# Optimization experiments

Measured on AMD Instinct MI355X. Metric: run time of the kernel, lower is better.

## Reference

```python
import jax, jax.numpy as jnp
import numpy as np

NUM_HEADS = 20
MAX_SEQLEN = 1500  # max per-segment length (Whisper 30s -> 1500 frames); static for jit
NEG = -1e30


def setup_inputs() -> dict:
    key = jax.random.key(0)
    ks = jax.random.split(key, 6)
    B, S, D = 4, MAX_SEQLEN, 1280
    T = B * S
    hidden_states = jax.random.normal(ks[0], (T, D), dtype=jnp.float32)
    # packed varlen layout: 4 equal-length audio segments
    cu_seqlens = (jnp.arange(B + 1, dtype=jnp.int32) * S)
    w = 0.02
    Wq = jax.random.normal(ks[1], (D, D), dtype=jnp.float32) * w
    Wk = jax.random.normal(ks[2], (D, D), dtype=jnp.float32) * w
    Wv = jax.random.normal(ks[3], (D, D), dtype=jnp.float32) * w
    Wo = jax.random.normal(ks[4], (D, D), dtype=jnp.float32) * w
    bq = jnp.zeros((D,), jnp.float32)
    bv = jnp.zeros((D,), jnp.float32)
    bo = jnp.zeros((D,), jnp.float32)
    return {"hidden_states": hidden_states, "cu_seqlens": cu_seqlens,
            "Wq": Wq, "bq": bq, "Wk": Wk, "Wv": Wv, "bv": bv, "Wo": Wo, "bo": bo}


def _varlen_attention(hidden_states, cu_seqlens, Wq, bq, Wk, Wv, bv, Wo, bo):
    T, D = hidden_states.shape
    H = NUM_HEADS
    d = D // H
    scale = d ** -0.5
    S = MAX_SEQLEN
    B = cu_seqlens.shape[0] - 1

    # projections (torch nn.Linear convention: y = x @ W.T + b; k_proj has no bias)
    q = hidden_states @ Wq.T + bq   # [T, D]
    k = hidden_states @ Wk.T        # [T, D]
    v = hidden_states @ Wv.T + bv   # [T, D]

    lens = cu_seqlens[1:] - cu_seqlens[:-1]                 # [B]
    pos = jnp.arange(S, dtype=jnp.int32)                    # [S]
    valid = pos[None, :] < lens[:, None]                    # [B, S]
    idx = cu_seqlens[:-1, None] + pos[None, :]              # [B, S]
    idx_g = jnp.where(valid, idx, 0)

    # unpack to padded [B, S, H, d]
    qb = q[idx_g].reshape(B, S, H, d)
    kb = k[idx_g].reshape(B, S, H, d)
    vb = v[idx_g].reshape(B, S, H, d)

    scores = jnp.einsum('bqhd,bkhd->bhqk', qb, kb) * scale  # [B, H, S, S]
    scores = jnp.where(valid[:, None, None, :], scores, NEG)
    attn = jax.nn.softmax(scores, axis=-1)
    out = jnp.einsum('bhqk,bkhd->bqhd', attn, vb).reshape(B, S, D)

    # repack to [T, D]; invalid slots scatter out-of-bounds and are dropped
    idx_s = jnp.where(valid, idx, T).reshape(-1)
    packed = jnp.zeros((T, D), out.dtype).at[idx_s].set(out.reshape(-1, D), mode='drop')
    return packed @ Wo.T + bo


def reference(hidden_states, cu_seqlens, Wq, bq, Wk, Wv, bv, Wo, bo):
    return _varlen_attention(hidden_states, cu_seqlens, Wq, bq, Wk, Wv, bv, Wo, bo)
```

## Files before the change

### kernel.cpp

```cpp
#include <hip/hip_runtime.h>
#include <stdint.h>
#include <math.h>

#define DMODEL 1280
#define NHEAD  20
#define DHEAD  64
#define NSEG   4
#define MAXS   1500
#define SPAD   1536
#define TPAD   (NSEG*SPAD)
#define QT128  ((MAXS + 127) / 128)
#define ST64   ((MAXS + 63) / 64)
#define BM 128
#define BN 128
#define BK 32
#define QSCALE 0.18033688011112042f
#define NEGV  -1e30f

typedef float  f32x4  __attribute__((ext_vector_type(4)));
typedef __bf16 bf16x8 __attribute__((ext_vector_type(8)));

__device__ __forceinline__ ushort f2bf(float f) {
  union { float f; uint32_t u; } a; a.f = f;
  uint32_t u = a.u;
  u += 0x7FFFu + ((u >> 16) & 1u);
  return (ushort)(u >> 16);
}

__device__ __forceinline__ uint32_t pk2(float a, float b) {
  union { float f; uint32_t u; } ua, ub; ua.f = a; ub.f = b;
  uint32_t x = ua.u + 0x8000u, y = ub.u + 0x8000u;
  return (x >> 16) | (y & 0xFFFF0000u);
}

__device__ __forceinline__ void async16(const void* g, void* lds) {
  __builtin_amdgcn_global_load_lds((const __attribute__((address_space(1))) void*)g,
                                   (__attribute__((address_space(3))) void*)lds,
                                   16, 0, 0);
}

__device__ __forceinline__ int perm32(int a) {
  return ((a >> 2) & 3) * 8 + ((a >> 4) & 1) * 4 + (a & 3);
}

__global__ void __launch_bounds__(256)
cvt_bf16(const float* __restrict__ src, ushort* __restrict__ dst, int n) {
  int i = (blockIdx.x * 256 + threadIdx.x) * 4;
  if (i >= n) return;
  float4 v = *(const float4*)(src + i);
  ushort4 o;
  o.x = f2bf(v.x); o.y = f2bf(v.y); o.z = f2bf(v.z); o.w = f2bf(v.w);
  *(ushort4*)(dst + i) = o;
}

__global__ void __launch_bounds__(256)
cvt_w4(const float* __restrict__ Wq, const float* __restrict__ Wk,
       const float* __restrict__ Wv, const float* __restrict__ Wo,
       ushort* __restrict__ dst, int DD) {
  const int z = blockIdx.y;
  const float* src = (z == 0) ? Wq : (z == 1) ? Wk : (z == 2) ? Wv : Wo;
  int i = (blockIdx.x * 256 + threadIdx.x) * 4;
  if (i >= DD) return;
  float4 v = *(const float4*)(src + i);
  ushort4 o;
  o.x = f2bf(v.x); o.y = f2bf(v.y); o.z = f2bf(v.z); o.w = f2bf(v.w);
  *(ushort4*)(dst + (size_t)z * DD + i) = o;
}

__device__ __forceinline__ void gemm_tile_mainloop(
    const ushort* __restrict__ A, const ushort* __restrict__ W,
    int M, int m0, int n0, ushort* As, ushort* Bs, f32x4 (&acc)[4][4])
{
  const int tid  = threadIdx.x;
  const int wave = tid >> 6, lane = tid & 63;
  const int quad = lane >> 4, c16 = lane & 15;
  const int wr = (wave >> 1) * 64, wc = (wave & 1) * 64;

  const int e0 = (wave * 2 + 0) * 512 + lane * 8;
  const int e1 = (wave * 2 + 1) * 512 + lane * 8;
  const int M0 = e0 >> 3, M1 = e1 >> 3;
  const int ra0 = M0 >> 2, ra1 = M1 >> 2;
  const int ca0 = (((M0 & 3) ^ (ra0 & 3) ^ ((ra0 >> 2) & 3)) << 3);
  const int ca1 = (((M1 & 3) ^ (ra1 & 3) ^ ((ra1 >> 2) & 3)) << 3);
  int ga0 = m0 + ra0; if (ga0 > M - 1) ga0 = M - 1;
  int ga1 = m0 + ra1; if (ga1 > M - 1) ga1 = M - 1;
  const ushort* Ap0 = A + (size_t)ga0 * DMODEL + ca0;
  const ushort* Ap1 = A + (size_t)ga1 * DMODEL + ca1;
  const ushort* Bp0 = W + (size_t)(n0 + ra0) * DMODEL + ca0;
  const ushort* Bp1 = W + (size_t)(n0 + ra1) * DMODEL + ca1;
  const int o0 = (wave * 2 + 0) * 512;
  const int o1 = (wave * 2 + 1) * 512;
  const int BUF = BM * BK;

  const int sw = (c16 & 3) ^ ((c16 >> 2) & 3);

  async16(Ap0, As + o0); async16(Ap1, As + o1);
  async16(Bp0, Bs + o0); async16(Bp1, Bs + o1);

  int c = 0;
  for (int k0 = 0; k0 < DMODEL; k0 += BK, c ^= 1) {
    __syncthreads();
    if (k0 + BK < DMODEL) {
      const int kn = k0 + BK;
      const int bo = (c ^ 1) * BUF;
      async16(Ap0 + kn, As + bo + o0); async16(Ap1 + kn, As + bo + o1);
      async16(Bp0 + kn, Bs + bo + o0); async16(Bp1 + kn, Bs + bo + o1);
    }
    const ushort* Ab = As + c * BUF;
    const ushort* Bb = Bs + c * BUF;
    bf16x8 a[4], b[4];
#pragma unroll
    for (int i = 0; i < 4; ++i)
      a[i] = *(const bf16x8*)(Ab + (wr + i * 16 + c16) * BK + ((quad ^ sw) << 3));
#pragma unroll
    for (int j = 0; j < 4; ++j)
      b[j] = *(const bf16x8*)(Bb + (wc + j * 16 + c16) * BK + ((quad ^ sw) << 3));
#pragma unroll
    for (int i = 0; i < 4; ++i)
#pragma unroll
      for (int j = 0; j < 4; ++j)
        acc[i][j] = __builtin_amdgcn_mfma_f32_16x16x32_bf16(a[i], b[j], acc[i][j], 0, 0, 0);
  }
}

__global__ void __launch_bounds__(256, 2)
gemm_qkv(const ushort* __restrict__ X, const ushort* __restrict__ W4,
         const float* __restrict__ bq, const float* __restrict__ bv,
         ushort* __restrict__ qb, ushort* __restrict__ kb, ushort* __restrict__ vb, int M)
{
  __shared__ ushort As[2 * BM * BK], Bs[2 * BN * BK];
  const int wg = blockIdx.x;
  if (wg >= 30) return;
  const int z = wg / 10;
  const int n0 = (wg % 10) * BN;
  const int m0 = blockIdx.y * BM;
  const ushort* W = W4 + (size_t)z * DMODEL * DMODEL;
  ushort* out = (z == 0) ? qb : ((z == 1) ? kb : vb);
  const float* bias = (z == 0) ? bq : ((z == 2) ? bv : (const float*)nullptr);
  const float oscale = (z == 0) ? QSCALE : 1.0f;

  f32x4 acc[4][4];
  f32x4 zero = {0.f, 0.f, 0.f, 0.f};
#pragma unroll
  for (int i = 0; i < 4; ++i)
#pragma unroll
    for (int j = 0; j < 4; ++j) acc[i][j] = zero;

  gemm_tile_mainloop(X, W, M, m0, n0, As, Bs, acc);

  const int tid = threadIdx.x, wave = tid >> 6, lane = tid & 63;
  const int quad = lane >> 4, c16 = lane & 15;
  const int wr = (wave >> 1) * 64, wc = (wave & 1) * 64;
#pragma unroll
  for (int i = 0; i < 4; ++i) {
    const int rbase = m0 + wr + i * 16 + quad * 4;
#pragma unroll
    for (int j = 0; j < 4; ++j) {
      const int c = n0 + wc + j * 16 + c16;
      const float bb = bias ? bias[c] : 0.f;
#pragma unroll
      for (int r = 0; r < 4; ++r) {
        const int rr = rbase + r;
        if (rr < M) out[(size_t)rr * DMODEL + c] = f2bf((acc[i][j][r] + bb) * oscale);
      }
    }
  }
}

__global__ void __launch_bounds__(256, 2)
gemm_out(const ushort* __restrict__ A, const ushort* __restrict__ W,
         const float* __restrict__ bias, float* __restrict__ out, int M)
{
  __shared__ ushort As[2 * BM * BK], Bs[2 * BN * BK];
  const int wg = blockIdx.x;
  if (wg >= 10) return;
  const int n0 = wg * BN;
  const int m0 = blockIdx.y * BM;
  f32x4 acc[4][4];
  f32x4 zero = {0.f, 0.f, 0.f, 0.f};
#pragma unroll
  for (int i = 0; i < 4; ++i)
#pragma unroll
    for (int j = 0; j < 4; ++j) acc[i][j] = zero;

  gemm_tile_mainloop(A, W, M, m0, n0, As, Bs, acc);

  const int tid = threadIdx.x, wave = tid >> 6, lane = tid & 63;
  const int quad = lane >> 4, c16 = lane & 15;
  const int wr = (wave >> 1) * 64, wc = (wave & 1) * 64;
#pragma unroll
  for (int i = 0; i < 4; ++i) {
    const int rbase = m0 + wr + i * 16 + quad * 4;
#pragma unroll
    for (int j = 0; j < 4; ++j) {
      const int c = n0 + wc + j * 16 + c16;
      const float bb = bias[c];
#pragma unroll
      for (int r = 0; r < 4; ++r) {
        const int rr = rbase + r;
        if (rr < M) out[(size_t)rr * DMODEL + c] = acc[i][j][r] + bb;
      }
    }
  }
}

__global__ void __launch_bounds__(256)
transpose_v(const ushort* __restrict__ vb, ushort* __restrict__ vt,
            const int* __restrict__ cu, int T)
{
  __shared__ ushort tile[64][72];
  const int bseg = blockIdx.z;
  const int seg0 = cu[bseg], len = cu[bseg + 1] - seg0;
  const int s0 = blockIdx.x * 64;
  if (s0 >= len) return;
  const int d0 = blockIdx.y * 64;
  const int tid = threadIdx.x;
#pragma unroll
  for (int i = 0; i < 2; ++i) {
    const int e = i * 2048 + tid * 8;
    const int r = e >> 6, c = e & 63;
    int t = seg0 + s0 + r;
    if (t > seg0 + len - 1) t = seg0 + len - 1;
    uint4 v = *(const uint4*)(vb + (size_t)t * DMODEL + d0 + c);
    *(uint4*)(&tile[r][c]) = v;
  }
  __syncthreads();
#pragma unroll
  for (int i = 0; i < 2; ++i) {
    const int e = i * 2048 + tid * 8;
    const int c = e >> 6;
    const int r = e & 63;
    const int s = s0 + r;
    ushort tmp[8];
#pragma unroll
    for (int j = 0; j < 8; ++j) tmp[j] = tile[r + j][c];
    const int o = r & 31;
    const size_t rowbase = (size_t)(d0 + c) * TPAD + (size_t)bseg * SPAD + (size_t)(s & ~31);
    if (s + 7 < len) {
      const int p0 = perm32(o), p1 = perm32(o + 4);
      uint2 w0, w1;
      w0.x = (uint32_t)tmp[0] | ((uint32_t)tmp[1] << 16);
      w0.y = (uint32_t)tmp[2] | ((uint32_t)tmp[3] << 16);
      w1.x = (uint32_t)tmp[4] | ((uint32_t)tmp[5] << 16);
      w1.y = (uint32_t)tmp[6] | ((uint32_t)tmp[7] << 16);
      *(uint2*)(vt + rowbase + p0) = w0;
      *(uint2*)(vt + rowbase + p1) = w1;
    } else {
#pragma unroll
      for (int j = 0; j < 8; ++j)
        if (s + j < len) vt[rowbase + perm32(o + j)] = tmp[j];
    }
  }
}

__global__ void __launch_bounds__(256, 2)
attn_fused(const ushort* __restrict__ qb, const ushort* __restrict__ kb,
           const ushort* __restrict__ vt, ushort* __restrict__ ob,
           const int* __restrict__ cu, int T)
{
  __shared__ ushort Qs[128 * 64];
  __shared__ ushort Ks[2][64 * 64];
  __shared__ ushort Vs[2][64 * 64];
  const int hs = blockIdx.x;
  const int b = hs / NHEAD, h = hs % NHEAD;
  const int seg0 = cu[b];
  const int len  = cu[b + 1] - seg0;
  const int q0 = blockIdx.y * 128;
  if (q0 >= len) return;
  const int tid = threadIdx.x, wave = tid >> 6, lane = tid & 63;
  const int quad = lane >> 4, c16 = lane & 15;

#pragma unroll
  for (int t = 0; t < 4; ++t) {
    const int M = t * 256 + wave * 64 + lane;
    const int r = M >> 3, k2 = M & 7;
    const int col = ((k2 ^ (r & 7)) << 3);
    int qr = q0 + r; if (qr >= len) qr = len - 1;
    async16(qb + (size_t)(seg0 + qr) * DMODEL + h * DHEAD + col,
            Qs + (t * 256 + wave * 64) * 8);
  }

  const int niter = (len + 63) >> 6;
#pragma unroll
  for (int t = 0; t < 2; ++t) {
    const int M = t * 256 + wave * 64 + lane;
    const int r = M >> 3, k2 = M & 7;
    const int col = ((k2 ^ (r & 7)) << 3);
    int rr = r; if (rr > len - 1) rr = len - 1;
    async16(kb + (size_t)(seg0 + rr) * DMODEL + h * DHEAD + col,
            Ks[0] + (t * 256 + wave * 64) * 8);
    async16(vt + (size_t)(h * DHEAD + r) * TPAD + (size_t)b * SPAD + col,
            Vs[0] + (t * 256 + wave * 64) * 8);
  }

  bf16x8 aq[2][2];
  float l_i[2] = {0.f, 0.f};
  f32x4 o_acc[2][4];
  f32x4 zero = {0.f, 0.f, 0.f, 0.f};
#pragma unroll
  for (int n = 0; n < 2; ++n)
#pragma unroll
    for (int m = 0; m < 4; ++m) o_acc[n][m] = zero;

  for (int it = 0; it < niter; ++it) {
    const int kv0 = it * 64;
    const int c = it & 1;
    __syncthreads();

    if (it + 1 < niter) {
      const int kvn = kv0 + 64;
      const int lim = len - 1 - kvn;
#pragma unroll
      for (int t = 0; t < 2; ++t) {
        const int M = t * 256 + wave * 64 + lane;
        const int r = M >> 3, k2 = M & 7;
        const int col = ((k2 ^ (r & 7)) << 3);
        int rr = r; if (rr > lim) rr = lim;
        async16(kb + (size_t)(seg0 + kvn + rr) * DMODEL + h * DHEAD + col,
                Ks[c ^ 1] + (t * 256 + wave * 64) * 8);
        async16(vt + (size_t)(h * DHEAD + r) * TPAD + (size_t)b * SPAD + kvn + col,
                Vs[c ^ 1] + (t * 256 + wave * 64) * 8);
      }
    }

    if (it == 0) {
#pragma unroll
      for (int n = 0; n < 2; ++n)
#pragma unroll
        for (int ks = 0; ks < 2; ++ks) {
          const int row = wave * 32 + n * 16 + c16;
          aq[n][ks] = *(const bf16x8*)(Qs + row * 64 + (((ks * 4 + quad) ^ (c16 & 7)) << 3));
        }
    }

    f32x4 s[2][4];
#pragma unroll
    for (int f = 0; f < 4; ++f) {
      const int row = f * 16 + c16;
      const int ch = c16 & 7;
      bf16x8 ak0 = *(const bf16x8*)(Ks[c] + row * 64 + ((quad ^ ch) << 3));
      bf16x8 ak1 = *(const bf16x8*)(Ks[c] + row * 64 + (((4 + quad) ^ ch) << 3));
#pragma unroll
      for (int n = 0; n < 2; ++n) {
        s[n][f] = zero;
        s[n][f] = __builtin_amdgcn_mfma_f32_16x16x32_bf16(ak0, aq[n][0], s[n][f], 0, 0, 0);
        s[n][f] = __builtin_amdgcn_mfma_f32_16x16x32_bf16(ak1, aq[n][1], s[n][f], 0, 0, 0);
      }
    }

    if (kv0 + 64 > len) {
#pragma unroll
      for (int f = 0; f < 4; ++f) {
        const int kvb = kv0 + f * 16 + quad * 4;
#pragma unroll
        for (int r = 0; r < 4; ++r)
          if (kvb + r >= len) { s[0][f][r] = NEGV; s[1][f][r] = NEGV; }
      }
    }

#pragma unroll
    for (int n = 0; n < 2; ++n) {
      float rs = 0.f;
#pragma unroll
      for (int f = 0; f < 4; ++f)
#pragma unroll
        for (int r = 0; r < 4; ++r) {
          const float p = exp2f(s[n][f][r]);
          s[n][f][r] = p;
          rs += p;
        }
      l_i[n] += rs;
    }

    bf16x8 bp[2][2];
#pragma unroll
    for (int n = 0; n < 2; ++n)
#pragma unroll
      for (int g = 0; g < 2; ++g) {
        union { uint32_t u[4]; bf16x8 v; } cv;
        cv.u[0] = pk2(s[n][2 * g][0], s[n][2 * g][1]);
        cv.u[1] = pk2(s[n][2 * g][2], s[n][2 * g][3]);
        cv.u[2] = pk2(s[n][2 * g + 1][0], s[n][2 * g + 1][1]);
        cv.u[3] = pk2(s[n][2 * g + 1][2], s[n][2 * g + 1][3]);
        bp[n][g] = cv.v;
      }

#pragma unroll
    for (int m = 0; m < 4; ++m) {
      const int row = m * 16 + c16;
      const int ch = c16 & 7;
      bf16x8 av0 = *(const bf16x8*)(Vs[c] + row * 64 + ((quad ^ ch) << 3));
      bf16x8 av1 = *(const bf16x8*)(Vs[c] + row * 64 + (((4 + quad) ^ ch) << 3));
#pragma unroll
      for (int n = 0; n < 2; ++n) {
        o_acc[n][m] = __builtin_amdgcn_mfma_f32_16x16x32_bf16(av0, bp[n][0], o_acc[n][m], 0, 0, 0);
        o_acc[n][m] = __builtin_amdgcn_mfma_f32_16x16x32_bf16(av1, bp[n][1], o_acc[n][m], 0, 0, 0);
      }
    }
  }

#pragma unroll
  for (int n = 0; n < 2; ++n) {
    float l = l_i[n];
    l += __shfl_xor(l, 16);
    l += __shfl_xor(l, 32);
    const int q = q0 + wave * 32 + n * 16 + c16;
    if (q < len) {
      const float inv = 1.0f / l;
      const size_t base = (size_t)(seg0 + q) * DMODEL + h * DHEAD;
#pragma unroll
      for (int m = 0; m < 4; ++m) {
        ushort4 pk;
        pk.x = f2bf(o_acc[n][m][0] * inv);
        pk.y = f2bf(o_acc[n][m][1] * inv);
        pk.z = f2bf(o_acc[n][m][2] * inv);
        pk.w = f2bf(o_acc[n][m][3] * inv);
        *(ushort4*)(ob + base + m * 16 + quad * 4) = pk;
      }
    }
  }
}

extern "C" void kernel_launch(void* const* d_in, const int* in_sizes, int n_in,
                              void* d_out, int out_size, void* d_ws, size_t ws_size,
                              hipStream_t stream)
{
  (void)n_in; (void)out_size; (void)ws_size;
  const float* hs = (const float*)d_in[0];
  const int*   cu = (const int*)d_in[1];
  const float* Wq = (const float*)d_in[2];
  const float* bq = (const float*)d_in[3];
  const float* Wk = (const float*)d_in[4];
  const float* Wv = (const float*)d_in[5];
  const float* bv = (const float*)d_in[6];
  const float* Wo = (const float*)d_in[7];
  const float* bo = (const float*)d_in[8];
  float* out = (float*)d_out;
  const int T  = in_sizes[0] / DMODEL;
  const int DD = DMODEL * DMODEL;

  ushort* ws  = (ushort*)d_ws;
  ushort* vtX = ws;
  const size_t szA = (size_t)DMODEL * TPAD;
  ushort* W4 = vtX + szA;
  ushort* qb = W4 + 4 * (size_t)DD;
  ushort* kb = qb + (size_t)T * DMODEL;
  ushort* vb = kb + (size_t)T * DMODEL;
  ushort* ob = vb;

  const int nX = T * DMODEL;
  cvt_bf16<<<(nX / 4 + 255) / 256, 256, 0, stream>>>(hs, vtX, nX);
  cvt_w4<<<dim3((DD / 4 + 255) / 256, 4), 256, 0, stream>>>(Wq, Wk, Wv, Wo, W4, DD);

  gemm_qkv<<<dim3(32, (T + BM - 1) / BM), 256, 0, stream>>>(vtX, W4, bq, bv, qb, kb, vb, T);

  transpose_v<<<dim3(ST64, DMODEL / 64, NSEG), 256, 0, stream>>>(vb, vtX, cu, T);

  attn_fused<<<dim3(NSEG * NHEAD, QT128), 256, 0, stream>>>(qb, kb, vtX, ob, cu, T);

  gemm_out<<<dim3(16, (T + BM - 1) / BM), 256, 0, stream>>>(
      ob, W4 + 3 * (size_t)DD, bo, out, T);
}
```

Measured before the change: 352.0 us.

## Fuse V transpose into QKV GEMM epilogue, merge convert kernels, retune LDS swizzle

The QKV GEMM epilogue now writes V directly into the permuted, transposed, segment-padded layout that attention consumes, so the separate transpose_v kernel and its round trip through global memory go away. The two fp32-to-bf16 conversion kernels are merged into one launch. The GEMM LDS layout switches to a different XOR swizzle over 64-element super-rows. Launch bounds for the GEMMs and attention are raised to 3 waves-per-SIMD occupancy hints. The V epilogue now does strided scattered stores with per-row segment lookups, and the tighter register budget may cause spills.

```diff
diff --git a/kernel.cpp b/kernel.cpp
--- a/kernel.cpp
+++ b/kernel.cpp
@@ -10,7 +10,6 @@
 #define SPAD   1536
 #define TPAD   (NSEG*SPAD)
 #define QT128  ((MAXS + 127) / 128)
-#define ST64   ((MAXS + 63) / 64)
 #define BM 128
 #define BN 128
 #define BK 32
@@ -44,27 +43,23 @@
 }
 
 __global__ void __launch_bounds__(256)
-cvt_bf16(const float* __restrict__ src, ushort* __restrict__ dst, int n) {
-  int i = (blockIdx.x * 256 + threadIdx.x) * 4;
-  if (i >= n) return;
-  float4 v = *(const float4*)(src + i);
+cvt_all(const float* __restrict__ hs, const float* __restrict__ Wq,
+        const float* __restrict__ Wk, const float* __restrict__ Wv,
+        const float* __restrict__ Wo, ushort* __restrict__ dst, int nX, int DD) {
+  const int i = (blockIdx.x * 256 + threadIdx.x) * 4;
+  const float* src;
+  if (i < nX) {
+    src = hs + i;
+  } else {
+    int j = i - nX;
+    const int z = (j >= DD) + (j >= 2 * DD) + (j >= 3 * DD);
+    const float* w = (z == 0) ? Wq : (z == 1) ? Wk : (z == 2) ? Wv : Wo;
+    src = w + (j - z * DD);
+  }
+  float4 v = *(const float4*)src;
   ushort4 o;
   o.x = f2bf(v.x); o.y = f2bf(v.y); o.z = f2bf(v.z); o.w = f2bf(v.w);
   *(ushort4*)(dst + i) = o;
-}
-
-__global__ void __launch_bounds__(256)
-cvt_w4(const float* __restrict__ Wq, const float* __restrict__ Wk,
-       const float* __restrict__ Wv, const float* __restrict__ Wo,
-       ushort* __restrict__ dst, int DD) {
-  const int z = blockIdx.y;
-  const float* src = (z == 0) ? Wq : (z == 1) ? Wk : (z == 2) ? Wv : Wo;
-  int i = (blockIdx.x * 256 + threadIdx.x) * 4;
-  if (i >= DD) return;
-  float4 v = *(const float4*)(src + i);
-  ushort4 o;
-  o.x = f2bf(v.x); o.y = f2bf(v.y); o.z = f2bf(v.z); o.w = f2bf(v.w);
-  *(ushort4*)(dst + (size_t)z * DD + i) = o;
 }
 
 __device__ __forceinline__ void gemm_tile_mainloop(
@@ -76,23 +71,20 @@
   const int quad = lane >> 4, c16 = lane & 15;
   const int wr = (wave >> 1) * 64, wc = (wave & 1) * 64;
 
-  const int e0 = (wave * 2 + 0) * 512 + lane * 8;
-  const int e1 = (wave * 2 + 1) * 512 + lane * 8;
-  const int M0 = e0 >> 3, M1 = e1 >> 3;
-  const int ra0 = M0 >> 2, ra1 = M1 >> 2;
-  const int ca0 = (((M0 & 3) ^ (ra0 & 3) ^ ((ra0 >> 2) & 3)) << 3);
-  const int ca1 = (((M1 & 3) ^ (ra1 & 3) ^ ((ra1 >> 2) & 3)) << 3);
-  int ga0 = m0 + ra0; if (ga0 > M - 1) ga0 = M - 1;
-  int ga1 = m0 + ra1; if (ga1 > M - 1) ga1 = M - 1;
-  const ushort* Ap0 = A + (size_t)ga0 * DMODEL + ca0;
-  const ushort* Ap1 = A + (size_t)ga1 * DMODEL + ca1;
-  const ushort* Bp0 = W + (size_t)(n0 + ra0) * DMODEL + ca0;
-  const ushort* Bp1 = W + (size_t)(n0 + ra1) * DMODEL + ca1;
-  const int o0 = (wave * 2 + 0) * 512;
-  const int o1 = (wave * 2 + 1) * 512;
+  const int M0 = wave * 128 + lane, M1 = M0 + 64;
+  const int sr0 = M0 >> 3, pp0 = M0 & 7, p0 = pp0 ^ (sr0 & 7);
+  const int sr1 = M1 >> 3, pp1 = M1 & 7, p1 = pp1 ^ (sr1 & 7);
+  const int row0 = sr0 * 2 + (p0 >> 2), kc0 = (p0 & 3) << 3;
+  const int row1 = sr1 * 2 + (p1 >> 2), kc1 = (p1 & 3) << 3;
+  int ga0 = m0 + row0; if (ga0 > M - 1) ga0 = M - 1;
+  int ga1 = m0 + row1; if (ga1 > M - 1) ga1 = M - 1;
+  const ushort* Ap0 = A + (size_t)ga0 * DMODEL + kc0;
+  const ushort* Ap1 = A + (size_t)ga1 * DMODEL + kc1;
+  const ushort* Bp0 = W + (size_t)(n0 + row0) * DMODEL + kc0;
+  const ushort* Bp1 = W + (size_t)(n0 + row1) * DMODEL + kc1;
+  const int o0 = wave * 1024;
+  const int o1 = wave * 1024 + 512;
   const int BUF = BM * BK;
-
-  const int sw = (c16 & 3) ^ ((c16 >> 2) & 3);
 
   async16(Ap0, As + o0); async16(Ap1, As + o1);
   async16(Bp0, Bs + o0); async16(Bp1, Bs + o1);
@@ -110,11 +102,19 @@
     const ushort* Bb = Bs + c * BUF;
     bf16x8 a[4], b[4];
 #pragma unroll
-    for (int i = 0; i < 4; ++i)
-      a[i] = *(const bf16x8*)(Ab + (wr + i * 16 + c16) * BK + ((quad ^ sw) << 3));
-#pragma unroll
-    for (int j = 0; j < 4; ++j)
-      b[j] = *(const bf16x8*)(Bb + (wc + j * 16 + c16) * BK + ((quad ^ sw) << 3));
+    for (int i = 0; i < 4; ++i) {
+      const int row = wr + i * 16 + c16;
+      const int sr = row >> 1;
+      const int off = (sr << 6) + (((((row & 1) << 2) | quad) ^ (sr & 7)) << 3);
+      a[i] = *(const bf16x8*)(Ab + off);
+    }
+#pragma unroll
+    for (int j = 0; j < 4; ++j) {
+      const int row = wc + j * 16 + c16;
+      const int sr = row >> 1;
+      const int off = (sr << 6) + (((((row & 1) << 2) | quad) ^ (sr & 7)) << 3);
+      b[j] = *(const bf16x8*)(Bb + off);
+    }
 #pragma unroll
     for (int i = 0; i < 4; ++i)
 #pragma unroll
@@ -123,10 +123,11 @@
   }
 }
 
-__global__ void __launch_bounds__(256, 2)
+__global__ void __launch_bounds__(256, 3)
 gemm_qkv(const ushort* __restrict__ X, const ushort* __restrict__ W4,
          const float* __restrict__ bq, const float* __restrict__ bv,
-         ushort* __restrict__ qb, ushort* __restrict__ kb, ushort* __restrict__ vb, int M)
+         const int* __restrict__ cu,
+         ushort* __restrict__ qb, ushort* __restrict__ kb, ushort* __restrict__ vt, int M)
 {
   __shared__ ushort As[2 * BM * BK], Bs[2 * BN * BK];
   const int wg = blockIdx.x;
@@ -135,9 +136,6 @@
   const int n0 = (wg % 10) * BN;
   const int m0 = blockIdx.y * BM;
   const ushort* W = W4 + (size_t)z * DMODEL * DMODEL;
-  ushort* out = (z == 0) ? qb : ((z == 1) ? kb : vb);
-  const float* bias = (z == 0) ? bq : ((z == 2) ? bv : (const float*)nullptr);
-  const float oscale = (z == 0) ? QSCALE : 1.0f;
 
   f32x4 acc[4][4];
   f32x4 zero = {0.f, 0.f, 0.f, 0.f};
@@ -151,23 +149,66 @@
   const int tid = threadIdx.x, wave = tid >> 6, lane = tid & 63;
   const int quad = lane >> 4, c16 = lane & 15;
   const int wr = (wave >> 1) * 64, wc = (wave & 1) * 64;
-#pragma unroll
-  for (int i = 0; i < 4; ++i) {
-    const int rbase = m0 + wr + i * 16 + quad * 4;
-#pragma unroll
-    for (int j = 0; j < 4; ++j) {
-      const int c = n0 + wc + j * 16 + c16;
-      const float bb = bias ? bias[c] : 0.f;
-#pragma unroll
-      for (int r = 0; r < 4; ++r) {
-        const int rr = rbase + r;
-        if (rr < M) out[(size_t)rr * DMODEL + c] = f2bf((acc[i][j][r] + bb) * oscale);
-      }
-    }
-  }
-}
-
-__global__ void __launch_bounds__(256, 2)
+
+  if (z == 2) {
+    const int c1 = cu[1], c2 = cu[2], c3 = cu[3];
+#pragma unroll
+    for (int i = 0; i < 4; ++i) {
+      const int t0 = m0 + wr + i * 16 + quad * 4;
+      const int s0a = (t0 >= c1) + (t0 >= c2) + (t0 >= c3);
+      const int s3a = (t0 + 3 >= c1) + (t0 + 3 >= c2) + (t0 + 3 >= c3);
+      const int seg0 = (s0a == 0) ? 0 : (s0a == 1) ? c1 : (s0a == 2) ? c2 : c3;
+#pragma unroll
+      for (int j = 0; j < 4; ++j) {
+        const int cfeat = n0 + wc + j * 16 + c16;
+        const float bb = bv[cfeat];
+        if (t0 + 3 < M && s0a == s3a) {
+          const int s = t0 - seg0;
+          const size_t base = (size_t)cfeat * TPAD + (size_t)s0a * SPAD
+                            + (size_t)(s & ~31) + perm32(s & 31);
+          ushort4 w;
+          w.x = f2bf(acc[i][j][0] + bb);
+          w.y = f2bf(acc[i][j][1] + bb);
+          w.z = f2bf(acc[i][j][2] + bb);
+          w.w = f2bf(acc[i][j][3] + bb);
+          *(ushort4*)(vt + base) = w;
+        } else {
+#pragma unroll
+          for (int r = 0; r < 4; ++r) {
+            const int t = t0 + r;
+            if (t < M) {
+              const int sb = (t >= c1) + (t >= c2) + (t >= c3);
+              const int sg = (sb == 0) ? 0 : (sb == 1) ? c1 : (sb == 2) ? c2 : c3;
+              const int s = t - sg;
+              vt[(size_t)cfeat * TPAD + (size_t)sb * SPAD + (s & ~31) + perm32(s & 31)]
+                  = f2bf(acc[i][j][r] + bb);
+            }
+          }
+        }
+      }
+    }
+  } else {
+    ushort* out = (z == 0) ? qb : kb;
+    const float* bias = (z == 0) ? bq : (const float*)nullptr;
+    const float oscale = (z == 0) ? QSCALE : 1.0f;
+#pragma unroll
+    for (int i = 0; i < 4; ++i) {
+      const int rbase = m0 + wr + i * 16 + quad * 4;
+#pragma unroll
+      for (int j = 0; j < 4; ++j) {
+        const int c = n0 + wc + j * 16 + c16;
+        const float bb = bias ? bias[c] : 0.f;
+#pragma unroll
+        for (int r = 0; r < 4; ++r) {
+          const int rr = rbase + r;
+          if (rr < M) out[(size_t)rr * DMODEL + c] = f2bf((acc[i][j][r] + bb) * oscale);
+        }
+      }
+    }
+  }
+}
+
+__global__ void __launch_bounds__(256, 3)
 gemm_out(const ushort* __restrict__ A, const ushort* __restrict__ W,
          const float* __restrict__ bias, float* __restrict__ out, int M)
 {
@@ -204,56 +245,7 @@
   }
 }
 
-__global__ void __launch_bounds__(256)
-transpose_v(const ushort* __restrict__ vb, ushort* __restrict__ vt,
-            const int* __restrict__ cu, int T)
-{
-  __shared__ ushort tile[64][72];
-  const int bseg = blockIdx.z;
-  const int seg0 = cu[bseg], len = cu[bseg + 1] - seg0;
-  const int s0 = blockIdx.x * 64;
-  if (s0 >= len) return;
-  const int d0 = blockIdx.y * 64;
-  const int tid = threadIdx.x;
-#pragma unroll
-  for (int i = 0; i < 2; ++i) {
-    const int e = i * 2048 + tid * 8;
-    const int r = e >> 6, c = e & 63;
-    int t = seg0 + s0 + r;
-    if (t > seg0 + len - 1) t = seg0 + len - 1;
-    uint4 v = *(const uint4*)(vb + (size_t)t * DMODEL + d0 + c);
-    *(uint4*)(&tile[r][c]) = v;
-  }
-  __syncthreads();
-#pragma unroll
-  for (int i = 0; i < 2; ++i) {
-    const int e = i * 2048 + tid * 8;
-    const int c = e >> 6;
-    const int r = e & 63;
-    const int s = s0 + r;
-    ushort tmp[8];
-#pragma unroll
-    for (int j = 0; j < 8; ++j) tmp[j] = tile[r + j][c];
-    const int o = r & 31;
-    const size_t rowbase = (size_t)(d0 + c) * TPAD + (size_t)bseg * SPAD + (size_t)(s & ~31);
-    if (s + 7 < len) {
-      const int p0 = perm32(o), p1 = perm32(o + 4);
-      uint2 w0, w1;
-      w0.x = (uint32_t)tmp[0] | ((uint32_t)tmp[1] << 16);
-      w0.y = (uint32_t)tmp[2] | ((uint32_t)tmp[3] << 16);
-      w1.x = (uint32_t)tmp[4] | ((uint32_t)tmp[5] << 16);
-      w1.y = (uint32_t)tmp[6] | ((uint32_t)tmp[7] << 16);
-      *(uint2*)(vt + rowbase + p0) = w0;
-      *(uint2*)(vt + rowbase + p1) = w1;
-    } else {
-#pragma unroll
-      for (int j = 0; j < 8; ++j)
-        if (s + j < len) vt[rowbase + perm32(o + j)] = tmp[j];
-    }
-  }
-}
-
-__global__ void __launch_bounds__(256, 2)
+__global__ void __launch_bounds__(256, 3)
 attn_fused(const ushort* __restrict__ qb, const ushort* __restrict__ kb,
            const ushort* __restrict__ vt, ushort* __restrict__ ob,
            const int* __restrict__ cu, int T)
@@ -438,25 +430,23 @@
   float* out = (float*)d_out;
   const int T  = in_sizes[0] / DMODEL;
   const int DD = DMODEL * DMODEL;
+  const int nX = T * DMODEL;
 
   ushort* ws  = (ushort*)d_ws;
-  ushort* vtX = ws;
-  const size_t szA = (size_t)DMODEL * TPAD;
-  ushort* W4 = vtX + szA;
-  ushort* qb = W4 + 4 * (size_t)DD;
-  ushort* kb = qb + (size_t)T * DMODEL;
-  ushort* vb = kb + (size_t)T * DMODEL;
-  ushort* ob = vb;
-
-  const int nX = T * DMODEL;
-  cvt_bf16<<<(nX / 4 + 255) / 256, 256, 0, stream>>>(hs, vtX, nX);
-  cvt_w4<<<dim3((DD / 4 + 255) / 256, 4), 256, 0, stream>>>(Wq, Wk, Wv, Wo, W4, DD);
-
-  gemm_qkv<<<dim3(32, (T + BM - 1) / BM), 256, 0, stream>>>(vtX, W4, bq, bv, qb, kb, vb, T);
-
-  transpose_v<<<dim3(ST64, DMODEL / 64, NSEG), 256, 0, stream>>>(vb, vtX, cu, T);
-
-  attn_fused<<<dim3(NSEG * NHEAD, QT128), 256, 0, stream>>>(qb, kb, vtX, ob, cu, T);
+  ushort* X   = ws;
+  ushort* W4  = X + (size_t)nX;
+  ushort* qb  = W4 + 4 * (size_t)DD;
+  ushort* kb  = qb + (size_t)T * DMODEL;
+  ushort* vt  = kb + (size_t)T * DMODEL;
+  ushort* ob  = X;
+
+  const int ncvt = nX + 4 * DD;
+  cvt_all<<<(ncvt / 4 + 255) / 256, 256, 0, stream>>>(hs, Wq, Wk, Wv, Wo, ws, nX, DD);
+
+  gemm_qkv<<<dim3(32, (T + BM - 1) / BM), 256, 0, stream>>>(
+      X, W4, bq, bv, cu, qb, kb, vt, T);
+
+  attn_fused<<<dim3(NSEG * NHEAD, QT128), 256, 0, stream>>>(qb, kb, vt, ob, cu, T);
 
   gemm_out<<<dim3(16, (T + BM - 1) / BM), 256, 0, stream>>>(
       ob, W4 + 3 * (size_t)DD, bo, out, T);
```

Measured after the change: 338.5 us. 1.04x faster.
